# Performance work log

Measured on AMD Instinct MI355X. Metric: run time of the kernel, lower is better.

## Reference

```python
import jax, jax.numpy as jnp
import numpy as np

GRAY_LEVELS = 16
DISTANCE = 1
ANGLES = (0, 45, 90, 135)


def _glcm_entropy(img):
    """img: [H, W] float in [0,1). Returns scalar entropy of the pooled GLCM."""
    L = GRAY_LEVELS
    d = DISTANCE
    # torch does (img * (L-1)).to(uint8): truncation toward zero for non-negative inputs
    q = (img * (L - 1)).astype(jnp.int32)  # [H, W], values in [0, L-1]
    counts = jnp.zeros((L * L,), jnp.float32)
    for angle in ANGLES:  # small fixed loop over 4 angles
        if angle == 0:
            s = jnp.roll(q, d, axis=1)
        elif angle == 45:
            s = jnp.roll(q, (d, -d), axis=(0, 1))
        elif angle == 90:
            s = jnp.roll(q, d, axis=0)
        elif angle == 135:
            s = jnp.roll(q, (d, d), axis=(0, 1))
        else:
            raise ValueError('Unsupported angle.')
        # fused scatter-add histogram over joint (i, j) bins, replaces L^2 mask-sums
        idx = (q * L + s).reshape(-1)  # [H*W]
        counts = counts.at[idx].add(1.0)
    glcm = counts / counts.sum()
    return -jnp.sum(glcm * jnp.log(glcm + 1e-10))


def setup_inputs() -> dict:
    key = jax.random.key(0)
    x = jax.random.uniform(key, (8, 16, 512, 512), dtype=jnp.float32)
    return {"x": x}


def reference(x):
    B, C, H, W = x.shape
    ent = jax.vmap(_glcm_entropy)(x.reshape(B * C, H, W))  # [B*C]
    # each (b,c) slice of the output is filled with that image's scalar entropy
    return jnp.broadcast_to(ent.reshape(B, C, 1, 1), (B, C, H, W))
```

## Files before the change

### kernel.cpp

```cpp
#include <hip/hip_runtime.h>
#include <math.h>

#define GLCM_L   16
#define IMG_H    512
#define IMG_W    512
#define N_IMG    128
#define STRIPS   8
#define ROWS_PER_STRIP (IMG_H / STRIPS)
#define NBINS    256

__global__ __launch_bounds__(256) void glcm_hist_kernel(
    const float* __restrict__ x, unsigned int* __restrict__ hist) {

    __shared__ unsigned int lh[4][NBINS];
    const int tid  = threadIdx.x;
    const int wave = tid >> 6;
    const int img  = blockIdx.y;
    const int strip = blockIdx.x;

    for (int i = tid; i < 4 * NBINS; i += 256) ((unsigned int*)lh)[i] = 0u;
    __syncthreads();

    const float* __restrict__ base = x + (size_t)img * (IMG_H * IMG_W);
    unsigned int* mh = lh[wave];

    const int half = tid >> 7;
    const int jj   = (tid & 127) << 2;
    const int jm1  = (jj + IMG_W - 1) & (IMG_W - 1);
    const int jp4  = (jj + 4) & (IMG_W - 1);
    const int rowBase = strip * ROWS_PER_STRIP;

    for (int it = 0; it < ROWS_PER_STRIP / 2; ++it) {
        const int r  = rowBase + it * 2 + half;
        const int ru = (r + IMG_H - 1) & (IMG_H - 1);

        const float4 c4 = *reinterpret_cast<const float4*>(base + (size_t)r  * IMG_W + jj);
        const float4 u4 = *reinterpret_cast<const float4*>(base + (size_t)ru * IMG_W + jj);
        const float  cm1 = base[(size_t)r  * IMG_W + jm1];
        const float  um1 = base[(size_t)ru * IMG_W + jm1];
        const float  up4 = base[(size_t)ru * IMG_W + jp4];

        int qc[5];
        int qu[6];
        qc[0] = (int)(cm1 * 15.0f);
        qc[1] = (int)(c4.x * 15.0f); qc[2] = (int)(c4.y * 15.0f);
        qc[3] = (int)(c4.z * 15.0f); qc[4] = (int)(c4.w * 15.0f);
        qu[0] = (int)(um1 * 15.0f);
        qu[1] = (int)(u4.x * 15.0f); qu[2] = (int)(u4.y * 15.0f);
        qu[3] = (int)(u4.z * 15.0f); qu[4] = (int)(u4.w * 15.0f);
        qu[5] = (int)(up4 * 15.0f);

        #pragma unroll
        for (int k = 0; k < 4; ++k) {
            const int q = qc[k + 1] << 4;
            atomicAdd(&mh[q + qc[k]],     1u);
            atomicAdd(&mh[q + qu[k + 2]], 1u);
            atomicAdd(&mh[q + qu[k + 1]], 1u);
            atomicAdd(&mh[q + qu[k]],     1u);
        }
    }

    __syncthreads();
    const unsigned int total = lh[0][tid] + lh[1][tid] + lh[2][tid] + lh[3][tid];
    atomicAdd(&hist[img * NBINS + tid], total);
}

__global__ __launch_bounds__(256) void glcm_entropy_kernel(
    const unsigned int* __restrict__ hist, float* __restrict__ ent) {

    __shared__ float partial[4];
    const int img = blockIdx.x;
    const int tid = threadIdx.x;

    const float c = (float)hist[img * NBINS + tid];
    const float p = c * (1.0f / 1048576.0f);
    float t = p * logf(p + 1e-10f);

    #pragma unroll
    for (int off = 32; off > 0; off >>= 1) t += __shfl_down(t, off, 64);
    if ((tid & 63) == 0) partial[tid >> 6] = t;
    __syncthreads();
    if (tid == 0) ent[img] = -(partial[0] + partial[1] + partial[2] + partial[3]);
}

__global__ __launch_bounds__(256) void glcm_fill_kernel(
    const float* __restrict__ ent, float4* __restrict__ out) {

    const int n4 = N_IMG * IMG_H * IMG_W / 4;
    const int stride = gridDim.x * 256;
    for (int v = blockIdx.x * 256 + threadIdx.x; v < n4; v += stride) {
        const float e = ent[v >> 16];
        out[v] = make_float4(e, e, e, e);
    }
}

extern "C" void kernel_launch(void* const* d_in, const int* in_sizes, int n_in,
                              void* d_out, int out_size, void* d_ws, size_t ws_size,
                              hipStream_t stream) {
    const float* x = (const float*)d_in[0];
    float4* out4 = reinterpret_cast<float4*>(d_out);

    unsigned int* hist = (unsigned int*)d_ws;
    float* ent = (float*)((char*)d_ws + (size_t)N_IMG * NBINS * sizeof(unsigned int));

    (void)hipMemsetAsync(d_ws, 0, (size_t)N_IMG * NBINS * sizeof(unsigned int), stream);

    glcm_hist_kernel<<<dim3(STRIPS, N_IMG), 256, 0, stream>>>(x, hist);
    glcm_entropy_kernel<<<N_IMG, 256, 0, stream>>>(hist, ent);
    glcm_fill_kernel<<<2048, 256, 0, stream>>>(ent, out4);
}
```

Baseline: 74.20 us.

## Fuse histogram, entropy and fill kernels via last-block ticket and flag spin

```diff
diff --git a/kernel.cpp b/kernel.cpp
--- a/kernel.cpp
+++ b/kernel.cpp
@@ -1,36 +1,44 @@
 #include <hip/hip_runtime.h>
 #include <math.h>
 
-#define GLCM_L   16
 #define IMG_H    512
 #define IMG_W    512
+#define IMG_HW   (IMG_H * IMG_W)
 #define N_IMG    128
 #define STRIPS   8
-#define ROWS_PER_STRIP (IMG_H / STRIPS)
 #define NBINS    256
 
-__global__ __launch_bounds__(256) void glcm_hist_kernel(
-    const float* __restrict__ x, unsigned int* __restrict__ hist) {
+typedef float f32x4 __attribute__((ext_vector_type(4)));
+
+__global__ __launch_bounds__(256) void glcm_fused_kernel(
+    const float* __restrict__ x, float* __restrict__ out,
+    unsigned int* __restrict__ hist, unsigned int* __restrict__ done,
+    unsigned int* __restrict__ flag) {
 
     __shared__ unsigned int lh[4][NBINS];
-    const int tid  = threadIdx.x;
-    const int wave = tid >> 6;
-    const int img  = blockIdx.y;
-    const int strip = blockIdx.x;
+    __shared__ float partial[4];
+    __shared__ unsigned int ticket_s;
+    __shared__ float ent_s;
+
+    const int tid   = threadIdx.x;
+    const int wave  = tid >> 6;
+    const int bid   = blockIdx.x;
+    const int img   = bid >> 3;
+    const int strip = bid & 7;
 
     for (int i = tid; i < 4 * NBINS; i += 256) ((unsigned int*)lh)[i] = 0u;
     __syncthreads();
 
-    const float* __restrict__ base = x + (size_t)img * (IMG_H * IMG_W);
+    const float* __restrict__ base = x + (size_t)img * IMG_HW;
     unsigned int* mh = lh[wave];
 
     const int half = tid >> 7;
     const int jj   = (tid & 127) << 2;
     const int jm1  = (jj + IMG_W - 1) & (IMG_W - 1);
     const int jp4  = (jj + 4) & (IMG_W - 1);
-    const int rowBase = strip * ROWS_PER_STRIP;
+    const int rowBase = strip * (IMG_H / STRIPS);
 
-    for (int it = 0; it < ROWS_PER_STRIP / 2; ++it) {
+    for (int it = 0; it < (IMG_H / STRIPS) / 2; ++it) {
         const int r  = rowBase + it * 2 + half;
         const int ru = (r + IMG_H - 1) & (IMG_H - 1);
 
@@ -63,49 +71,60 @@
     __syncthreads();
     const unsigned int total = lh[0][tid] + lh[1][tid] + lh[2][tid] + lh[3][tid];
     atomicAdd(&hist[img * NBINS + tid], total);
-}
+    __threadfence();
+    __syncthreads();
+    if (tid == 0) ticket_s = atomicAdd(&done[img], 1u);
+    __syncthreads();
 
-__global__ __launch_bounds__(256) void glcm_entropy_kernel(
-    const unsigned int* __restrict__ hist, float* __restrict__ ent) {
+    if (ticket_s == 7u) {
+        __threadfence();
+        const unsigned int c = __hip_atomic_load(&hist[img * NBINS + tid],
+                                                 __ATOMIC_RELAXED,
+                                                 __HIP_MEMORY_SCOPE_AGENT);
+        const float p = (float)c * (1.0f / 1048576.0f);
+        float t = p * logf(p + 1e-10f);
+        #pragma unroll
+        for (int off = 32; off > 0; off >>= 1) t += __shfl_down(t, off, 64);
+        if ((tid & 63) == 0) partial[wave] = t;
+        __syncthreads();
+        if (tid == 0) {
+            const float e = -(partial[0] + partial[1] + partial[2] + partial[3]);
+            __hip_atomic_store(&flag[img], __float_as_uint(e),
+                               __ATOMIC_RELEASE, __HIP_MEMORY_SCOPE_AGENT);
+        }
+    }
 
-    __shared__ float partial[4];
-    const int img = blockIdx.x;
-    const int tid = threadIdx.x;
+    if (tid == 0) {
+        unsigned int fb;
+        while ((fb = __hip_atomic_load(&flag[img], __ATOMIC_ACQUIRE,
+                                       __HIP_MEMORY_SCOPE_AGENT)) == 0u)
+            __builtin_amdgcn_s_sleep(2);
+        ent_s = __uint_as_float(fb);
+    }
+    __syncthreads();
 
-    const float c = (float)hist[img * NBINS + tid];
-    const float p = c * (1.0f / 1048576.0f);
-    float t = p * logf(p + 1e-10f);
-
-    #pragma unroll
-    for (int off = 32; off > 0; off >>= 1) t += __shfl_down(t, off, 64);
-    if ((tid & 63) == 0) partial[tid >> 6] = t;
-    __syncthreads();
-    if (tid == 0) ent[img] = -(partial[0] + partial[1] + partial[2] + partial[3]);
-}
-
-__global__ __launch_bounds__(256) void glcm_fill_kernel(
-    const float* __restrict__ ent, float4* __restrict__ out) {
-
-    const int n4 = N_IMG * IMG_H * IMG_W / 4;
-    const int stride = gridDim.x * 256;
-    for (int v = blockIdx.x * 256 + threadIdx.x; v < n4; v += stride) {
-        const float e = ent[v >> 16];
-        out[v] = make_float4(e, e, e, e);
-    }
+    const float e = ent_s;
+    const f32x4 v = {e, e, e, e};
+    f32x4* ob = reinterpret_cast<f32x4*>(out) +
+                (size_t)img * (IMG_HW / 4) + strip * (IMG_HW / 4 / STRIPS);
+    #pragma unroll 4
+    for (int i = tid; i < IMG_HW / 4 / STRIPS; i += 256)
+        __builtin_nontemporal_store(v, ob + i);
 }
 
 extern "C" void kernel_launch(void* const* d_in, const int* in_sizes, int n_in,
                               void* d_out, int out_size, void* d_ws, size_t ws_size,
                               hipStream_t stream) {
     const float* x = (const float*)d_in[0];
-    float4* out4 = reinterpret_cast<float4*>(d_out);
+    float* out = (float*)d_out;
 
     unsigned int* hist = (unsigned int*)d_ws;
-    float* ent = (float*)((char*)d_ws + (size_t)N_IMG * NBINS * sizeof(unsigned int));
+    unsigned int* done = hist + N_IMG * NBINS;
+    unsigned int* flag = done + N_IMG;
 
-    (void)hipMemsetAsync(d_ws, 0, (size_t)N_IMG * NBINS * sizeof(unsigned int), stream);
+    (void)hipMemsetAsync(d_ws, 0,
+                         (size_t)(N_IMG * NBINS + 2 * N_IMG) * sizeof(unsigned int),
+                         stream);
 
-    glcm_hist_kernel<<<dim3(STRIPS, N_IMG), 256, 0, stream>>>(x, hist);
-    glcm_entropy_kernel<<<N_IMG, 256, 0, stream>>>(hist, ent);
-    glcm_fill_kernel<<<2048, 256, 0, stream>>>(ent, out4);
+    glcm_fused_kernel<<<N_IMG * STRIPS, 256, 0, stream>>>(x, out, hist, done, flag);
 }
```

Result: slower. 258.7 us (+248.7%).
